# Optimization experiments

Measured on AMD Instinct MI355X. Metric: run time of the kernel, lower is better.

Reference implementation:

```python
import jax, jax.numpy as jnp
import numpy as np

# dims
B, T, N, D = 4, 256, 64, 512
H, DH = 8, 64            # n_head, d_head; H*DH == D
DF = 4 * D               # SwiGLU hidden
EPS = 1e-6


def rmsnorm(x, w):
    return x * jax.lax.rsqrt(jnp.mean(x * x, axis=-1, keepdims=True) + EPS) * w


def phi(x):
    # positive feature map for kernelized (linear) attention ('SMReg' assumed elu+1 style)
    return jax.nn.elu(x) + 1.0


def heads(x):
    return x.reshape(*x.shape[:-1], H, DH)


def lin_att(Xq, Xkv, wq, wk, wv, wo):
    # low-rank high-order linear attention: kernelized attention applied
    # independently along each tensor mode (time T, entities N), averaged.
    q = phi(heads(Xq @ wq))   # [B,T,N,H,DH]
    k = phi(heads(Xkv @ wk))
    v = heads(Xkv @ wv)
    # mode 1 (time): attend over T, batch over (B,N)
    kv_t = jnp.einsum('btnhk,btnhv->bnhkv', k, v)          # [B,N,H,DH,DH]
    ks_t = k.sum(axis=1)                                   # [B,N,H,DH]
    den_t = jnp.einsum('btnhk,bnhk->btnh', q, ks_t) + EPS
    out_t = jnp.einsum('btnhk,bnhkv->btnhv', q, kv_t) / den_t[..., None]
    # mode 2 (entities): attend over N, batch over (B,T)
    kv_n = jnp.einsum('btnhk,btnhv->bthkv', k, v)
    ks_n = k.sum(axis=2)
    den_n = jnp.einsum('btnhk,bthk->btnh', q, ks_n) + EPS
    out_n = jnp.einsum('btnhk,bthkv->btnhv', q, kv_n) / den_n[..., None]
    out = 0.5 * (out_t + out_n)
    return out.reshape(*Xq.shape[:-1], H * DH) @ wo


def swiglu(x, w1, w2, w3):
    return (jax.nn.silu(x @ w1) * (x @ w3)) @ w2


def setup_inputs() -> dict:
    key = jax.random.key(0)
    ks = jax.random.split(key, 20)
    s = 0.02
    inp = {
        'X': jax.random.normal(ks[0], (B, T, N, D), jnp.float32),
        'Z': jax.random.normal(ks[1], (B, T, N, D), jnp.float32),
        'n1': jnp.ones((D,), jnp.float32),
        'n2': jnp.ones((D,), jnp.float32),
        'n3': jnp.ones((D,), jnp.float32),
        'nz': jnp.ones((D,), jnp.float32),
        'a_wq': jax.random.normal(ks[2], (D, H * DH), jnp.float32) * s,
        'a_wk': jax.random.normal(ks[3], (D, H * DH), jnp.float32) * s,
        'a_wv': jax.random.normal(ks[4], (D, H * DH), jnp.float32) * s,
        'a_wo': jax.random.normal(ks[5], (H * DH, D), jnp.float32) * s,
        'c_wq': jax.random.normal(ks[6], (D, H * DH), jnp.float32) * s,
        'c_wk': jax.random.normal(ks[7], (D, H * DH), jnp.float32) * s,
        'c_wv': jax.random.normal(ks[8], (D, H * DH), jnp.float32) * s,
        'c_wo': jax.random.normal(ks[9], (H * DH, D), jnp.float32) * s,
        'f_w1': jax.random.normal(ks[10], (D, DF), jnp.float32) * s,
        'f_w2': jax.random.normal(ks[11], (DF, D), jnp.float32) * s,
        'f_w3': jax.random.normal(ks[12], (D, DF), jnp.float32) * s,
    }
    return inp


def reference(X, Z, n1, n2, n3, nz, a_wq, a_wk, a_wv, a_wo,
              c_wq, c_wk, c_wv, c_wo, f_w1, f_w2, f_w3):
    # h = X + SelfAtt(norm1(X))
    xn = rmsnorm(X, n1)
    h = X + lin_att(xn, xn, a_wq, a_wk, a_wv, a_wo)
    # h = h + CrossAtt(norm3(h), normz(Z))
    h = h + lin_att(rmsnorm(h, n3), rmsnorm(Z, nz), c_wq, c_wk, c_wv, c_wo)
    # out = h + SwiGLU(norm2(h))   (dropout p=0 -> identity)
    return h + swiglu(rmsnorm(h, n2), f_w1, f_w2, f_w3)
```

## Files before the change

kernel.cpp:

```cpp
#include <hip/hip_runtime.h>

typedef short s16x8 __attribute__((ext_vector_type(8)));
typedef float f32x4 __attribute__((ext_vector_type(4)));
typedef unsigned short u16;
typedef unsigned int u32;

__device__ __forceinline__ float bf2f(u16 u) {
  union { unsigned int i; float f; } v; v.i = ((unsigned int)u) << 16; return v.f;
}
__device__ __forceinline__ u16 f2bf(float f) {
  union { float f; unsigned int i; } v; v.f = f;
  unsigned int r = v.i + 0x7fffu + ((v.i >> 16) & 1u);
  return (u16)(r >> 16);
}

__device__ __forceinline__ void gload16(const u16* g, u16* l) {
  __builtin_amdgcn_global_load_lds(
      (const __attribute__((address_space(1))) u32*)g,
      (__attribute__((address_space(3))) u32*)l, 16, 0, 0);
}

template<int KDIM, int NDIM>
__launch_bounds__(256)
__global__ void wprep(const float* __restrict__ in, u16* __restrict__ out) {
  __shared__ float t[64][65];
  const int tid = threadIdx.x;
  const int nb = NDIM / 64;
  const int tk0 = (blockIdx.x / nb) * 64;
  const int tn0 = (blockIdx.x % nb) * 64;
#pragma unroll
  for (int i = 0; i < 16; i++) {
    int idx = i * 256 + tid;
    int r = idx >> 6, c = idx & 63;
    t[r][c] = in[(long)(tk0 + r) * NDIM + (tn0 + c)];
  }
  __syncthreads();
#pragma unroll
  for (int i = 0; i < 16; i++) {
    int idx = i * 256 + tid;
    int nn = idx >> 6, kk = idx & 63;
    out[(long)(tn0 + nn) * KDIM + (tk0 + kk)] = f2bf(t[kk][nn]);
  }
}

__launch_bounds__(256)
__global__ void rmsnorm_f32(const float* __restrict__ x, const float* __restrict__ w,
                            u16* __restrict__ out) {
  const long row = (long)blockIdx.x * 4 + (threadIdx.x >> 6);
  const int lane = threadIdx.x & 63;
  const float* xr = x + row * 512 + lane * 8;
  float4 v0 = *(const float4*)xr;
  float4 v1 = *(const float4*)(xr + 4);
  float ss = v0.x*v0.x + v0.y*v0.y + v0.z*v0.z + v0.w*v0.w
           + v1.x*v1.x + v1.y*v1.y + v1.z*v1.z + v1.w*v1.w;
#pragma unroll
  for (int o = 1; o < 64; o <<= 1) ss += __shfl_xor(ss, o);
  float sc = rsqrtf(ss * (1.0f / 512.0f) + 1e-6f);
  const float* wp = w + lane * 8;
  float4 w0 = *(const float4*)wp;
  float4 w1 = *(const float4*)(wp + 4);
  union { u16 u[8]; uint4 v; } o;
  o.u[0] = f2bf(v0.x * sc * w0.x);
  o.u[1] = f2bf(v0.y * sc * w0.y);
  o.u[2] = f2bf(v0.z * sc * w0.z);
  o.u[3] = f2bf(v0.w * sc * w0.w);
  o.u[4] = f2bf(v1.x * sc * w1.x);
  o.u[5] = f2bf(v1.y * sc * w1.y);
  o.u[6] = f2bf(v1.z * sc * w1.z);
  o.u[7] = f2bf(v1.w * sc * w1.w);
  *(uint4*)(out + row * 512 + lane * 8) = o.v;
}

__launch_bounds__(256)
__global__ void rmsnorm_bf16(const u16* __restrict__ x, const float* __restrict__ w,
                             u16* __restrict__ out) {
  const long row = (long)blockIdx.x * 4 + (threadIdx.x >> 6);
  const int lane = threadIdx.x & 63;
  uint4 u = *(const uint4*)(x + row * 512 + lane * 8);
  const u16* us = (const u16*)&u;
  float f[8];
  float ss = 0.f;
#pragma unroll
  for (int j = 0; j < 8; j++) { f[j] = bf2f(us[j]); ss += f[j] * f[j]; }
#pragma unroll
  for (int o = 1; o < 64; o <<= 1) ss += __shfl_xor(ss, o);
  float sc = rsqrtf(ss * (1.0f / 512.0f) + 1e-6f);
  const float* wp = w + lane * 8;
  union { u16 u[8]; uint4 v; } o;
#pragma unroll
  for (int j = 0; j < 8; j++) o.u[j] = f2bf(f[j] * sc * wp[j]);
  *(uint4*)(out + row * 512 + lane * 8) = o.v;
}

enum { EPI_BF16 = 0, EPI_PHI = 1, EPI_RESX = 2, EPI_RESH = 3, EPI_SILUMUL = 4,
       EPI_OUTF = 5, EPI_QKV = 6, EPI_KV = 7 };

template<int KD, int EPI>
__launch_bounds__(256)
__global__ void gemm128(const u16* __restrict__ A, const u16* __restrict__ Bt,
                        void* __restrict__ C0, void* __restrict__ C1,
                        void* __restrict__ C2, const void* __restrict__ aux,
                        int Ns) {
  __shared__ u16 As[2][128][64];
  __shared__ u16 Bs[2][128][64];
  const int tid = threadIdx.x;
  const int lane = tid & 63;
  const int wv = tid >> 6;
  const int gx = gridDim.x;
  int L = blockIdx.y * gx + blockIdx.x;
  const int cpx = (gx * gridDim.y) >> 3;
  L = (L & 7) * cpx + (L >> 3);
  const long m0 = (long)(L / gx) * 128;
  const int nb = L % gx;
  const long n0 = (long)nb * 128;

  const int wr = (wv >> 1) * 64;
  const int wc = (wv & 1) * 64;
  const int fr = lane & 15;
  const int frq = lane >> 4;

  const int r0 = wv * 32 + (lane >> 3);
  const int sg8 = ((lane & 7) ^ ((lane >> 3) & 7)) * 8;
  const u16* Ag = A + (m0 + r0) * KD + sg8;
  const u16* Bg = Bt + (n0 + r0) * KD + sg8;
  u16* Alds = &As[0][0][0] + wv * 2048;
  u16* Blds = &Bs[0][0][0] + wv * 2048;

  f32x4 acc[4][4] = {};

  auto STAGE = [&](int b, int kt) {
    const long k0 = (long)kt * 64;
#pragma unroll
    for (int j = 0; j < 4; j++) {
      gload16(Ag + (long)(j * 8) * KD + k0, Alds + b * 8192 + j * 512);
      gload16(Bg + (long)(j * 8) * KD + k0, Blds + b * 8192 + j * 512);
    }
  };
  auto COMPUTE = [&](int b) {
#pragma unroll
    for (int ks = 0; ks < 2; ks++) {
      const int slot = ((ks * 4 + frq) ^ (fr & 7)) * 8;
      s16x8 af[4], bf[4];
#pragma unroll
      for (int i = 0; i < 4; i++) af[i] = *(const s16x8*)&As[b][wr + i * 16 + fr][slot];
#pragma unroll
      for (int j = 0; j < 4; j++) bf[j] = *(const s16x8*)&Bs[b][wc + j * 16 + fr][slot];
#pragma unroll
      for (int i = 0; i < 4; i++)
#pragma unroll
        for (int j = 0; j < 4; j++)
          acc[i][j] = __builtin_amdgcn_mfma_f32_16x16x32_bf16(af[i], bf[j], acc[i][j], 0, 0, 0);
    }
  };

  constexpr int NT = KD / 64;
  STAGE(0, 0);
#pragma unroll 1
  for (int t = 0; t < NT; ++t) {
    if (t + 1 < NT) {
      STAGE((t + 1) & 1, t + 1);
      asm volatile("s_waitcnt vmcnt(8)" ::: "memory");
    } else {
      asm volatile("s_waitcnt vmcnt(0)" ::: "memory");
    }
    __builtin_amdgcn_s_barrier();
    COMPUTE(t & 1);
    asm volatile("s_waitcnt lgkmcnt(0)" ::: "memory");
    __builtin_amdgcn_s_barrier();
  }

  const int col = lane & 15;
  const int rb = frq * 4;
#pragma unroll
  for (int i = 0; i < 4; i++) {
#pragma unroll
    for (int r = 0; r < 4; r++) {
      long m = m0 + wr + i * 16 + rb + r;
#pragma unroll
      for (int j = 0; j < 4; j++) {
        long nlocal = wc + j * 16 + col;
        float v = acc[i][j][r];
        if constexpr (EPI == EPI_QKV) {
          int seg = nb >> 2;
          long off = m * 512 + ((n0 + nlocal) & 511);
          u16* P = (u16*)(seg == 0 ? C0 : (seg == 1 ? C1 : C2));
          float p = (seg < 2) ? (v > 0.f ? v + 1.f : __expf(v)) : v;
          P[off] = f2bf(p);
        } else if constexpr (EPI == EPI_KV) {
          int seg = nb >> 2;
          long off = m * 512 + ((n0 + nlocal) & 511);
          u16* P = (u16*)(seg == 0 ? C0 : C1);
          float p = (seg == 0) ? (v > 0.f ? v + 1.f : __expf(v)) : v;
          P[off] = f2bf(p);
        } else {
          long off = m * Ns + (n0 + nlocal);
          if constexpr (EPI == EPI_BF16) {
            ((u16*)C0)[off] = f2bf(v);
          } else if constexpr (EPI == EPI_PHI) {
            float p = v > 0.f ? v + 1.f : __expf(v);
            ((u16*)C0)[off] = f2bf(p);
          } else if constexpr (EPI == EPI_RESX) {
            ((u16*)C0)[off] = f2bf(((const float*)aux)[off] + v);
          } else if constexpr (EPI == EPI_RESH) {
            ((u16*)C0)[off] = f2bf(bf2f(((const u16*)aux)[off]) + v);
          } else if constexpr (EPI == EPI_SILUMUL) {
            float t2 = bf2f(((const u16*)aux)[off]);
            float s = t2 / (1.f + __expf(-t2));
            ((u16*)C0)[off] = f2bf(s * v);
          } else {
            ((float*)C0)[off] = bf2f(((const u16*)aux)[off]) + v;
          }
        }
      }
    }
  }
}

__launch_bounds__(256)
__global__ void att_mode1(const u16* __restrict__ q, const u16* __restrict__ k,
                          const u16* __restrict__ v, u16* __restrict__ attc) {
  __shared__ u16 Ks[128][72];
  __shared__ u16 Vs[128][72];
  __shared__ u16 KVT[64][72];
  __shared__ float ksump[4][64];
  __shared__ float ksum_s[64];
  __shared__ float dinv[256];
  const int tid = threadIdx.x;
  const int lane = tid & 63;
  const int w = tid >> 6;
  const int bnh = blockIdx.x;
  const int h = bnh & 7;
  const int bn = bnh >> 3;
  const int n = bn & 63;
  const int b = bn >> 6;
  const long base = ((long)b * 16384 + n) * 512 + h * 64;
  const int fr = lane & 15;
  const int fk = (lane >> 4) * 8;
  const int sdk = tid & 63, sqq = tid >> 6;

  f32x4 acc[4] = {};
  float ks_acc = 0.f;

  for (int half = 0; half < 2; half++) {
    __syncthreads();
#pragma unroll
    for (int rep = 0; rep < 4; rep++) {
      int idx = rep * 256 + tid;
      int tl = idx >> 3, c8 = idx & 7;
      long go = base + (long)(half * 128 + tl) * 32768 + c8 * 8;
      *(uint4*)&Ks[tl][c8 * 8] = *(const uint4*)(k + go);
      *(uint4*)&Vs[tl][c8 * 8] = *(const uint4*)(v + go);
    }
    __syncthreads();
#pragma unroll
    for (int i = 0; i < 32; i++) ks_acc += bf2f(Ks[sqq * 32 + i][sdk]);
#pragma unroll
    for (int ks = 0; ks < 4; ks++) {
      s16x8 af, bfr[4];
#pragma unroll
      for (int e = 0; e < 8; e++) af[e] = (short)Vs[ks * 32 + fk + e][w * 16 + fr];
#pragma unroll
      for (int j = 0; j < 4; j++)
#pragma unroll
        for (int e = 0; e < 8; e++) bfr[j][e] = (short)Ks[ks * 32 + fk + e][j * 16 + fr];
#pragma unroll
      for (int j = 0; j < 4; j++)
        acc[j] = __builtin_amdgcn_mfma_f32_16x16x32_bf16(af, bfr[j], acc[j], 0, 0, 0);
    }
  }
  ksump[sqq][sdk] = ks_acc;
  __syncthreads();
  {
    const int colL = lane & 15, rb = (lane >> 4) * 4;
#pragma unroll
    for (int j = 0; j < 4; j++)
#pragma unroll
      for (int r = 0; r < 4; r++)
        KVT[w * 16 + rb + r][j * 16 + colL] = f2bf(acc[j][r]);
  }
  if (tid < 64) ksum_s[tid] = ksump[0][tid] + ksump[1][tid] + ksump[2][tid] + ksump[3][tid];
  __syncthreads();
  {
    const u16* qp = q + base + (long)tid * 32768;
    float d = 0.f;
#pragma unroll
    for (int c8 = 0; c8 < 8; c8++) {
      uint4 u = ((const uint4*)qp)[c8];
      const u16* us = (const u16*)&u;
#pragma unroll
      for (int e = 0; e < 8; e++) d += bf2f(us[e]) * ksum_s[c8 * 8 + e];
    }
    dinv[tid] = 0.5f / (d + 1e-6f);
  }
  f32x4 acc2[4][4] = {};
#pragma unroll
  for (int ks = 0; ks < 2; ks++) {
    s16x8 aq[4], bk[4];
#pragma unroll
    for (int i = 0; i < 4; i++)
      aq[i] = *(const s16x8*)(q + base + (long)(w * 64 + i * 16 + fr) * 32768 + ks * 32 + fk);
#pragma unroll
    for (int j = 0; j < 4; j++)
      bk[j] = *(const s16x8*)&KVT[j * 16 + fr][ks * 32 + fk];
#pragma unroll
    for (int i = 0; i < 4; i++)
#pragma unroll
      for (int j = 0; j < 4; j++)
        acc2[i][j] = __builtin_amdgcn_mfma_f32_16x16x32_bf16(aq[i], bk[j], acc2[i][j], 0, 0, 0);
  }
  __syncthreads();
  const int colL = lane & 15, rb = (lane >> 4) * 4;
#pragma unroll
  for (int i = 0; i < 4; i++)
#pragma unroll
    for (int r = 0; r < 4; r++) {
      int t = w * 64 + i * 16 + rb + r;
      float inv = dinv[t];
#pragma unroll
      for (int j = 0; j < 4; j++)
        attc[base + (long)t * 32768 + j * 16 + colL] = f2bf(acc2[i][j][r] * inv);
    }
}

__launch_bounds__(256)
__global__ void att_mode2(const u16* __restrict__ q, const u16* __restrict__ k,
                          const u16* __restrict__ v, u16* __restrict__ attc) {
  __shared__ u16 Ks[64][72];
  __shared__ u16 Vs[64][72];
  __shared__ u16 KVT[64][72];
  __shared__ float ksump[4][64];
  __shared__ float ksum_s[64];
  __shared__ float dinv[64];
  const int tid = threadIdx.x;
  const int lane = tid & 63;
  const int w = tid >> 6;
  const int bth = blockIdx.x;
  const int h = bth & 7;
  const long bt = bth >> 3;
  const long base = bt * 32768 + h * 64;
  const int fr = lane & 15;
  const int fk = (lane >> 4) * 8;
  const int sdk = tid & 63, sqq = tid >> 6;

#pragma unroll
  for (int rep = 0; rep < 2; rep++) {
    int idx = rep * 256 + tid;
    int nl = idx >> 3, c8 = idx & 7;
    long go = base + (long)nl * 512 + c8 * 8;
    *(uint4*)&Ks[nl][c8 * 8] = *(const uint4*)(k + go);
    *(uint4*)&Vs[nl][c8 * 8] = *(const uint4*)(v + go);
  }
  __syncthreads();
  {
    float s = 0.f;
#pragma unroll
    for (int i = 0; i < 16; i++) s += bf2f(Ks[sqq * 16 + i][sdk]);
    ksump[sqq][sdk] = s;
  }
  f32x4 acc[4] = {};
#pragma unroll
  for (int ks = 0; ks < 2; ks++) {
    s16x8 af, bfr[4];
#pragma unroll
    for (int e = 0; e < 8; e++) af[e] = (short)Vs[ks * 32 + fk + e][w * 16 + fr];
#pragma unroll
    for (int j = 0; j < 4; j++)
#pragma unroll
      for (int e = 0; e < 8; e++) bfr[j][e] = (short)Ks[ks * 32 + fk + e][j * 16 + fr];
#pragma unroll
    for (int j = 0; j < 4; j++)
      acc[j] = __builtin_amdgcn_mfma_f32_16x16x32_bf16(af, bfr[j], acc[j], 0, 0, 0);
  }
  __syncthreads();
  {
    const int colL = lane & 15, rb = (lane >> 4) * 4;
#pragma unroll
    for (int j = 0; j < 4; j++)
#pragma unroll
      for (int r = 0; r < 4; r++)
        KVT[w * 16 + rb + r][j * 16 + colL] = f2bf(acc[j][r]);
  }
  if (tid < 64) ksum_s[tid] = ksump[0][tid] + ksump[1][tid] + ksump[2][tid] + ksump[3][tid];
  __syncthreads();
  if (tid < 64) {
    const u16* qp = q + base + (long)tid * 512;
    float d = 0.f;
#pragma unroll
    for (int c8 = 0; c8 < 8; c8++) {
      uint4 u = ((const uint4*)qp)[c8];
      const u16* us = (const u16*)&u;
#pragma unroll
      for (int e = 0; e < 8; e++) d += bf2f(us[e]) * ksum_s[c8 * 8 + e];
    }
    dinv[tid] = 0.5f / (d + 1e-6f);
  }
  f32x4 acc2[4] = {};
#pragma unroll
  for (int ks = 0; ks < 2; ks++) {
    s16x8 aq, bk[4];
    aq = *(const s16x8*)(q + base + (long)(w * 16 + fr) * 512 + ks * 32 + fk);
#pragma unroll
    for (int j = 0; j < 4; j++)
      bk[j] = *(const s16x8*)&KVT[j * 16 + fr][ks * 32 + fk];
#pragma unroll
    for (int j = 0; j < 4; j++)
      acc2[j] = __builtin_amdgcn_mfma_f32_16x16x32_bf16(aq, bk[j], acc2[j], 0, 0, 0);
  }
  __syncthreads();
  const int colL = lane & 15, rb = (lane >> 4) * 4;
#pragma unroll
  for (int r = 0; r < 4; r++) {
    int nr = w * 16 + rb + r;
    float inv = dinv[nr];
#pragma unroll
    for (int j = 0; j < 4; j++) {
      long o = base + (long)nr * 512 + j * 16 + colL;
      attc[o] = f2bf(bf2f(attc[o]) + acc2[j][r] * inv);
    }
  }
}

extern "C" void kernel_launch(void* const* d_in, const int* in_sizes, int n_in,
                              void* d_out, int out_size, void* d_ws, size_t ws_size,
                              hipStream_t stream) {
  const float* X    = (const float*)d_in[0];
  const float* Z    = (const float*)d_in[1];
  const float* n1   = (const float*)d_in[2];
  const float* n2   = (const float*)d_in[3];
  const float* n3   = (const float*)d_in[4];
  const float* nz   = (const float*)d_in[5];
  const float* a_wq = (const float*)d_in[6];
  const float* a_wk = (const float*)d_in[7];
  const float* a_wv = (const float*)d_in[8];
  const float* a_wo = (const float*)d_in[9];
  const float* c_wq = (const float*)d_in[10];
  const float* c_wk = (const float*)d_in[11];
  const float* c_wv = (const float*)d_in[12];
  const float* c_wo = (const float*)d_in[13];
  const float* f_w1 = (const float*)d_in[14];
  const float* f_w2 = (const float*)d_in[15];
  const float* f_w3 = (const float*)d_in[16];
  float* out = (float*)d_out;
  (void)ws_size; (void)in_sizes; (void)n_in; (void)out_size;

  char* p = (char*)d_ws;
  size_t off = 0;
  auto take = [&](size_t bytes) -> char* {
    char* r = p + off;
    off += (bytes + 255) & ~(size_t)255;
    return r;
  };
  u16* w_aq = (u16*)take(512 * 512 * 2);
  u16* w_ak = (u16*)take(512 * 512 * 2);
  u16* w_av = (u16*)take(512 * 512 * 2);
  u16* w_ao = (u16*)take(512 * 512 * 2);
  u16* w_cq = (u16*)take(512 * 512 * 2);
  u16* w_ck = (u16*)take(512 * 512 * 2);
  u16* w_cv = (u16*)take(512 * 512 * 2);
  u16* w_co = (u16*)take(512 * 512 * 2);
  u16* w_f1 = (u16*)take(2048 * 512 * 2);
  u16* w_f3 = (u16*)take(2048 * 512 * 2);
  u16* w_f2 = (u16*)take(512 * 2048 * 2);
  u16* xn   = (u16*)take((size_t)65536 * 512 * 2);
  u16* hbuf = (u16*)take((size_t)65536 * 512 * 2);
  u16* qbuf = (u16*)take((size_t)65536 * 512 * 2);
  u16* kbuf = (u16*)d_out;
  u16* vbuf = (u16*)d_out + (size_t)65536 * 512;
  u16* attc = xn;
  u16* tslot = qbuf;

  dim3 b256(256);
  dim3 gQKV(12, 512);
  dim3 gKV(8, 512);
  dim3 gP(4, 512);
  dim3 gU(16, 128);
  dim3 gD(4, 128);

  wprep<512, 512><<<64, b256, 0, stream>>>(a_wq, w_aq);
  wprep<512, 512><<<64, b256, 0, stream>>>(a_wk, w_ak);
  wprep<512, 512><<<64, b256, 0, stream>>>(a_wv, w_av);
  wprep<512, 512><<<64, b256, 0, stream>>>(a_wo, w_ao);
  wprep<512, 512><<<64, b256, 0, stream>>>(c_wq, w_cq);
  wprep<512, 512><<<64, b256, 0, stream>>>(c_wk, w_ck);
  wprep<512, 512><<<64, b256, 0, stream>>>(c_wv, w_cv);
  wprep<512, 512><<<64, b256, 0, stream>>>(c_wo, w_co);
  wprep<512, 2048><<<256, b256, 0, stream>>>(f_w1, w_f1);
  wprep<512, 2048><<<256, b256, 0, stream>>>(f_w3, w_f3);
  wprep<2048, 512><<<256, b256, 0, stream>>>(f_w2, w_f2);

  rmsnorm_f32<<<16384, b256, 0, stream>>>(X, n1, xn);
  gemm128<512, EPI_QKV><<<gQKV, b256, 0, stream>>>(xn, w_aq, qbuf, kbuf, vbuf, nullptr, 1536);
  att_mode1<<<2048, b256, 0, stream>>>(qbuf, kbuf, vbuf, attc);
  att_mode2<<<8192, b256, 0, stream>>>(qbuf, kbuf, vbuf, attc);
  gemm128<512, EPI_RESX><<<gP, b256, 0, stream>>>(attc, w_ao, hbuf, nullptr, nullptr, X, 512);

  rmsnorm_bf16<<<16384, b256, 0, stream>>>(hbuf, n3, xn);
  gemm128<512, EPI_PHI><<<gP, b256, 0, stream>>>(xn, w_cq, qbuf, nullptr, nullptr, nullptr, 512);
  rmsnorm_f32<<<16384, b256, 0, stream>>>(Z, nz, xn);
  gemm128<512, EPI_KV><<<gKV, b256, 0, stream>>>(xn, w_ck, kbuf, vbuf, nullptr, nullptr, 1024);
  att_mode1<<<2048, b256, 0, stream>>>(qbuf, kbuf, vbuf, attc);
  att_mode2<<<8192, b256, 0, stream>>>(qbuf, kbuf, vbuf, attc);
  gemm128<512, EPI_RESH><<<gP, b256, 0, stream>>>(attc, w_co, hbuf, nullptr, nullptr, hbuf, 512);

  rmsnorm_bf16<<<16384, b256, 0, stream>>>(hbuf, n2, xn);
  const int CH = 16384;
  for (int c = 0; c < 4; c++) {
    const size_t ro = (size_t)c * CH * 512;
    gemm128<512, EPI_BF16><<<gU, b256, 0, stream>>>(xn + ro, w_f1, tslot, nullptr, nullptr, nullptr, 2048);
    gemm128<512, EPI_SILUMUL><<<gU, b256, 0, stream>>>(xn + ro, w_f3, tslot, nullptr, nullptr, tslot, 2048);
    gemm128<2048, EPI_OUTF><<<gD, b256, 0, stream>>>(tslot, w_f2, out + ro, nullptr, nullptr, hbuf + ro, 512);
  }
}
```

Baseline: 1.498 ms.

## Enlarge GEMM tiles to 256x256 with 8 waves and 4-stage LDS pipeline

Replaces the 128x128 GEMM kernel (4 waves, 2-stage, K-step 64) with a 256x256 tile using 8 waves, each computing a 128x64 sub-tile, with a 4-buffer LDS ring and K-step 32 prefetched two stages ahead. The larger tile raises arithmetic intensity and cuts global/L2 traffic per FLOP, and s_setprio is raised around the MFMA block. In exchange it uses more accumulator registers (32 f32x4 per lane) and 64KB of LDS, which lowers occupancy and gives fewer workgroups per launch.

Result: slower. 1.771 ms (+18.2%).

```diff
diff --git a/kernel.cpp b/kernel.cpp
--- a/kernel.cpp
+++ b/kernel.cpp
@@ -96,98 +96,104 @@
        EPI_OUTF = 5, EPI_QKV = 6, EPI_KV = 7 };
 
 template<int KD, int EPI>
-__launch_bounds__(256)
-__global__ void gemm128(const u16* __restrict__ A, const u16* __restrict__ Bt,
+__launch_bounds__(512)
+__global__ void gemm256(const u16* __restrict__ A, const u16* __restrict__ Bt,
                         void* __restrict__ C0, void* __restrict__ C1,
                         void* __restrict__ C2, const void* __restrict__ aux,
                         int Ns) {
-  __shared__ u16 As[2][128][64];
-  __shared__ u16 Bs[2][128][64];
+  __shared__ u16 As[4][256][32];
+  __shared__ u16 Bs[4][256][32];
   const int tid = threadIdx.x;
   const int lane = tid & 63;
-  const int wv = tid >> 6;
+  const int wid = tid >> 6;
   const int gx = gridDim.x;
   int L = blockIdx.y * gx + blockIdx.x;
   const int cpx = (gx * gridDim.y) >> 3;
   L = (L & 7) * cpx + (L >> 3);
-  const long m0 = (long)(L / gx) * 128;
+  const long m0 = (long)(L / gx) * 256;
   const int nb = L % gx;
-  const long n0 = (long)nb * 128;
-
-  const int wr = (wv >> 1) * 64;
-  const int wc = (wv & 1) * 64;
+  const long n0 = (long)nb * 256;
+
+  const int wrbase = (wid >> 2) * 128;
+  const int wcbase = (wid & 3) * 64;
   const int fr = lane & 15;
   const int frq = lane >> 4;
 
-  const int r0 = wv * 32 + (lane >> 3);
-  const int sg8 = ((lane & 7) ^ ((lane >> 3) & 7)) * 8;
-  const u16* Ag = A + (m0 + r0) * KD + sg8;
-  const u16* Bg = Bt + (n0 + r0) * KD + sg8;
-  u16* Alds = &As[0][0][0] + wv * 2048;
-  u16* Blds = &Bs[0][0][0] + wv * 2048;
-
-  f32x4 acc[4][4] = {};
-
-  auto STAGE = [&](int b, int kt) {
-    const long k0 = (long)kt * 64;
-#pragma unroll
-    for (int j = 0; j < 4; j++) {
-      gload16(Ag + (long)(j * 8) * KD + k0, Alds + b * 8192 + j * 512);
-      gload16(Bg + (long)(j * 8) * KD + k0, Blds + b * 8192 + j * 512);
-    }
+  const int srow = lane >> 2;
+  const int sslot = ((lane & 3) ^ (srow & 3)) * 8;
+  const u16* Ag = A + (m0 + wid * 32 + srow) * KD + sslot;
+  const u16* Bg = Bt + (n0 + wid * 32 + srow) * KD + sslot;
+  u16* Al = &As[0][0][0] + wid * 1024;
+  u16* Bl = &Bs[0][0][0] + wid * 1024;
+
+  f32x4 acc[8][4] = {};
+
+  auto STAGE = [&](int t) {
+    const int b = t & 3;
+    const long k0 = (long)t * 32;
+    gload16(Ag + k0, Al + b * 8192);
+    gload16(Ag + (long)16 * KD + k0, Al + b * 8192 + 512);
+    gload16(Bg + k0, Bl + b * 8192);
+    gload16(Bg + (long)16 * KD + k0, Bl + b * 8192 + 512);
   };
   auto COMPUTE = [&](int b) {
-#pragma unroll
-    for (int ks = 0; ks < 2; ks++) {
-      const int slot = ((ks * 4 + frq) ^ (fr & 7)) * 8;
-      s16x8 af[4], bf[4];
-#pragma unroll
-      for (int i = 0; i < 4; i++) af[i] = *(const s16x8*)&As[b][wr + i * 16 + fr][slot];
-#pragma unroll
-      for (int j = 0; j < 4; j++) bf[j] = *(const s16x8*)&Bs[b][wc + j * 16 + fr][slot];
-#pragma unroll
-      for (int i = 0; i < 4; i++)
-#pragma unroll
-        for (int j = 0; j < 4; j++)
-          acc[i][j] = __builtin_amdgcn_mfma_f32_16x16x32_bf16(af[i], bf[j], acc[i][j], 0, 0, 0);
-    }
+    s16x8 af[8], bf[4];
+#pragma unroll
+    for (int i = 0; i < 8; i++) {
+      const int row = wrbase + i * 16 + fr;
+      af[i] = *(const s16x8*)&As[b][row][(frq ^ (row & 3)) * 8];
+    }
+#pragma unroll
+    for (int j = 0; j < 4; j++) {
+      const int row = wcbase + j * 16 + fr;
+      bf[j] = *(const s16x8*)&Bs[b][row][(frq ^ (row & 3)) * 8];
+    }
+    __builtin_amdgcn_s_setprio(1);
+#pragma unroll
+    for (int i = 0; i < 8; i++)
+#pragma unroll
+      for (int j = 0; j < 4; j++)
+        acc[i][j] = __builtin_amdgcn_mfma_f32_16x16x32_bf16(af[i], bf[j], acc[i][j], 0, 0, 0);
+    __builtin_amdgcn_s_setprio(0);
   };
 
-  constexpr int NT = KD / 64;
-  STAGE(0, 0);
+  constexpr int NT = KD / 32;
+  STAGE(0);
+  STAGE(1);
 #pragma unroll 1
   for (int t = 0; t < NT; ++t) {
-    if (t + 1 < NT) {
-      STAGE((t + 1) & 1, t + 1);
+    if (t + 2 < NT) {
+      STAGE(t + 2);
       asm volatile("s_waitcnt vmcnt(8)" ::: "memory");
+    } else if (t + 1 < NT) {
+      asm volatile("s_waitcnt vmcnt(4)" ::: "memory");
     } else {
       asm volatile("s_waitcnt vmcnt(0)" ::: "memory");
     }
     __builtin_amdgcn_s_barrier();
-    COMPUTE(t & 1);
-    asm volatile("s_waitcnt lgkmcnt(0)" ::: "memory");
+    COMPUTE(t & 3);
     __builtin_amdgcn_s_barrier();
   }
 
   const int col = lane & 15;
   const int rb = frq * 4;
 #pragma unroll
-  for (int i = 0; i < 4; i++) {
+  for (int i = 0; i < 8; i++) {
 #pragma unroll
     for (int r = 0; r < 4; r++) {
-      long m = m0 + wr + i * 16 + rb + r;
+      long m = m0 + wrbase + i * 16 + rb + r;
 #pragma unroll
       for (int j = 0; j < 4; j++) {
-        long nlocal = wc + j * 16 + col;
+        long nlocal = wcbase + j * 16 + col;
         float v = acc[i][j][r];
         if constexpr (EPI == EPI_QKV) {
-          int seg = nb >> 2;
+          int seg = nb >> 1;
           long off = m * 512 + ((n0 + nlocal) & 511);
           u16* P = (u16*)(seg == 0 ? C0 : (seg == 1 ? C1 : C2));
           float p = (seg < 2) ? (v > 0.f ? v + 1.f : __expf(v)) : v;
           P[off] = f2bf(p);
         } else if constexpr (EPI == EPI_KV) {
-          int seg = nb >> 2;
+          int seg = nb >> 1;
           long off = m * 512 + ((n0 + nlocal) & 511);
           u16* P = (u16*)(seg == 0 ? C0 : C1);
           float p = (seg == 0) ? (v > 0.f ? v + 1.f : __expf(v)) : v;
@@ -470,11 +476,12 @@
   u16* tslot = qbuf;
 
   dim3 b256(256);
-  dim3 gQKV(12, 512);
-  dim3 gKV(8, 512);
-  dim3 gP(4, 512);
-  dim3 gU(16, 128);
-  dim3 gD(4, 128);
+  dim3 b512(512);
+  dim3 gQKV(6, 256);
+  dim3 gKV(4, 256);
+  dim3 gP(2, 256);
+  dim3 gU(8, 64);
+  dim3 gD(2, 64);
 
   wprep<512, 512><<<64, b256, 0, stream>>>(a_wq, w_aq);
   wprep<512, 512><<<64, b256, 0, stream>>>(a_wk, w_ak);
@@ -489,25 +496,25 @@
   wprep<2048, 512><<<256, b256, 0, stream>>>(f_w2, w_f2);
 
   rmsnorm_f32<<<16384, b256, 0, stream>>>(X, n1, xn);
-  gemm128<512, EPI_QKV><<<gQKV, b256, 0, stream>>>(xn, w_aq, qbuf, kbuf, vbuf, nullptr, 1536);
+  gemm256<512, EPI_QKV><<<gQKV, b512, 0, stream>>>(xn, w_aq, qbuf, kbuf, vbuf, nullptr, 1536);
   att_mode1<<<2048, b256, 0, stream>>>(qbuf, kbuf, vbuf, attc);
   att_mode2<<<8192, b256, 0, stream>>>(qbuf, kbuf, vbuf, attc);
-  gemm128<512, EPI_RESX><<<gP, b256, 0, stream>>>(attc, w_ao, hbuf, nullptr, nullptr, X, 512);
+  gemm256<512, EPI_RESX><<<gP, b512, 0, stream>>>(attc, w_ao, hbuf, nullptr, nullptr, X, 512);
 
   rmsnorm_bf16<<<16384, b256, 0, stream>>>(hbuf, n3, xn);
-  gemm128<512, EPI_PHI><<<gP, b256, 0, stream>>>(xn, w_cq, qbuf, nullptr, nullptr, nullptr, 512);
+  gemm256<512, EPI_PHI><<<gP, b512, 0, stream>>>(xn, w_cq, qbuf, nullptr, nullptr, nullptr, 512);
   rmsnorm_f32<<<16384, b256, 0, stream>>>(Z, nz, xn);
-  gemm128<512, EPI_KV><<<gKV, b256, 0, stream>>>(xn, w_ck, kbuf, vbuf, nullptr, nullptr, 1024);
+  gemm256<512, EPI_KV><<<gKV, b512, 0, stream>>>(xn, w_ck, kbuf, vbuf, nullptr, nullptr, 1024);
   att_mode1<<<2048, b256, 0, stream>>>(qbuf, kbuf, vbuf, attc);
   att_mode2<<<8192, b256, 0, stream>>>(qbuf, kbuf, vbuf, attc);
-  gemm128<512, EPI_RESH><<<gP, b256, 0, stream>>>(attc, w_co, hbuf, nullptr, nullptr, hbuf, 512);
+  gemm256<512, EPI_RESH><<<gP, b512, 0, stream>>>(attc, w_co, hbuf, nullptr, nullptr, hbuf, 512);
 
   rmsnorm_bf16<<<16384, b256, 0, stream>>>(hbuf, n2, xn);
   const int CH = 16384;
   for (int c = 0; c < 4; c++) {
     const size_t ro = (size_t)c * CH * 512;
-    gemm128<512, EPI_BF16><<<gU, b256, 0, stream>>>(xn + ro, w_f1, tslot, nullptr, nullptr, nullptr, 2048);
-    gemm128<512, EPI_SILUMUL><<<gU, b256, 0, stream>>>(xn + ro, w_f3, tslot, nullptr, nullptr, tslot, 2048);
-    gemm128<2048, EPI_OUTF><<<gD, b256, 0, stream>>>(tslot, w_f2, out + ro, nullptr, nullptr, hbuf + ro, 512);
-  }
-}
+    gemm256<512, EPI_BF16><<<gU, b512, 0, stream>>>(xn + ro, w_f1, tslot, nullptr, nullptr, nullptr, 2048);
+    gemm256<512, EPI_SILUMUL><<<gU, b512, 0, stream>>>(xn + ro, w_f3, tslot, nullptr, nullptr, tslot, 2048);
+    gemm256<2048, EPI_OUTF><<<gD, b512, 0, stream>>>(tslot, w_f2, out + ro, nullptr, nullptr, hbuf + ro, 512);
+  }
+}
```

## Store K/V transposed and pair-packed in LDS for vectorized MFMA fragment loads

Applied to the files above, without the earlier changes.

In both attention kernels, K and V tiles are now transposed into LDS as u32 words, each packing two consecutive time or entity elements. MFMA operand fragments and the key-sum reductions can then use 128-bit LDS reads instead of eight scalar u16 gathers per fragment. Mode 1 now loads all 256 timesteps in one pass instead of two halves, which removes a sync loop but uses more LDS per block and may lower occupancy. The transposing scatter stores into LDS may cause bank conflicts.

New measurement: 1.518 ms. No clear change (+1.4%).

```diff
diff --git a/kernel.cpp b/kernel.cpp
--- a/kernel.cpp
+++ b/kernel.cpp
@@ -12,6 +12,12 @@
   union { float f; unsigned int i; } v; v.f = f;
   unsigned int r = v.i + 0x7fffu + ((v.i >> 16) & 1u);
   return (u16)(r >> 16);
+}
+__device__ __forceinline__ float bflo(u32 x) {
+  union { unsigned int i; float f; } v; v.i = x << 16; return v.f;
+}
+__device__ __forceinline__ float bfhi(u32 x) {
+  union { unsigned int i; float f; } v; v.i = x & 0xffff0000u; return v.f;
 }
 
 __device__ __forceinline__ void gload16(const u16* g, u16* l) {
@@ -219,8 +225,8 @@
 __launch_bounds__(256)
 __global__ void att_mode1(const u16* __restrict__ q, const u16* __restrict__ k,
                           const u16* __restrict__ v, u16* __restrict__ attc) {
-  __shared__ u16 Ks[128][72];
-  __shared__ u16 Vs[128][72];
+  __shared__ u32 KT[64][132];
+  __shared__ u32 VT[64][132];
   __shared__ u16 KVT[64][72];
   __shared__ float ksump[4][64];
   __shared__ float ksum_s[64];
@@ -235,43 +241,55 @@
   const int b = bn >> 6;
   const long base = ((long)b * 16384 + n) * 512 + h * 64;
   const int fr = lane & 15;
-  const int fk = (lane >> 4) * 8;
-  const int sdk = tid & 63, sqq = tid >> 6;
+  const int frq = lane >> 4;
+  const int fk = frq * 8;
+
+#pragma unroll
+  for (int r = 0; r < 4; r++) {
+    const int tp = (tid & 63) + (r & 1) * 64;
+    const int c8 = (tid >> 6) + (r >> 1) * 4;
+    const long g0 = base + (long)(2 * tp) * 32768 + c8 * 8;
+    uint4 ka = *(const uint4*)(k + g0);
+    uint4 kb = *(const uint4*)(k + g0 + 32768);
+    uint4 va = *(const uint4*)(v + g0);
+    uint4 vb = *(const uint4*)(v + g0 + 32768);
+    const u16* kap = (const u16*)&ka; const u16* kbp = (const u16*)&kb;
+    const u16* vap = (const u16*)&va; const u16* vbp = (const u16*)&vb;
+#pragma unroll
+    for (int e = 0; e < 8; e++) {
+      KT[c8 * 8 + e][tp] = (u32)kap[e] | ((u32)kbp[e] << 16);
+      VT[c8 * 8 + e][tp] = (u32)vap[e] | ((u32)vbp[e] << 16);
+    }
+  }
+  __syncthreads();
+
+  {
+    const int dk = tid >> 2, qq = tid & 3;
+    float s = 0.f;
+#pragma unroll
+    for (int i = 0; i < 8; i++) {
+      uint4 x = *(const uint4*)&KT[dk][qq * 32 + i * 4];
+      s += bflo(x.x) + bfhi(x.x) + bflo(x.y) + bfhi(x.y)
+         + bflo(x.z) + bfhi(x.z) + bflo(x.w) + bfhi(x.w);
+    }
+    ksump[qq][dk] = s;
+  }
 
   f32x4 acc[4] = {};
-  float ks_acc = 0.f;
-
-  for (int half = 0; half < 2; half++) {
-    __syncthreads();
-#pragma unroll
-    for (int rep = 0; rep < 4; rep++) {
-      int idx = rep * 256 + tid;
-      int tl = idx >> 3, c8 = idx & 7;
-      long go = base + (long)(half * 128 + tl) * 32768 + c8 * 8;
-      *(uint4*)&Ks[tl][c8 * 8] = *(const uint4*)(k + go);
-      *(uint4*)&Vs[tl][c8 * 8] = *(const uint4*)(v + go);
-    }
-    __syncthreads();
-#pragma unroll
-    for (int i = 0; i < 32; i++) ks_acc += bf2f(Ks[sqq * 32 + i][sdk]);
-#pragma unroll
-    for (int ks = 0; ks < 4; ks++) {
-      s16x8 af, bfr[4];
-#pragma unroll
-      for (int e = 0; e < 8; e++) af[e] = (short)Vs[ks * 32 + fk + e][w * 16 + fr];
-#pragma unroll
-      for (int j = 0; j < 4; j++)
-#pragma unroll
-        for (int e = 0; e < 8; e++) bfr[j][e] = (short)Ks[ks * 32 + fk + e][j * 16 + fr];
-#pragma unroll
-      for (int j = 0; j < 4; j++)
-        acc[j] = __builtin_amdgcn_mfma_f32_16x16x32_bf16(af, bfr[j], acc[j], 0, 0, 0);
-    }
-  }
-  ksump[sqq][sdk] = ks_acc;
+#pragma unroll
+  for (int ks = 0; ks < 8; ks++) {
+    s16x8 af = *(const s16x8*)&VT[w * 16 + fr][ks * 16 + frq * 4];
+    s16x8 bk[4];
+#pragma unroll
+    for (int j = 0; j < 4; j++)
+      bk[j] = *(const s16x8*)&KT[j * 16 + fr][ks * 16 + frq * 4];
+#pragma unroll
+    for (int j = 0; j < 4; j++)
+      acc[j] = __builtin_amdgcn_mfma_f32_16x16x32_bf16(af, bk[j], acc[j], 0, 0, 0);
+  }
   __syncthreads();
   {
-    const int colL = lane & 15, rb = (lane >> 4) * 4;
+    const int colL = lane & 15, rb = frq * 4;
 #pragma unroll
     for (int j = 0; j < 4; j++)
 #pragma unroll
@@ -309,7 +327,7 @@
         acc2[i][j] = __builtin_amdgcn_mfma_f32_16x16x32_bf16(aq[i], bk[j], acc2[i][j], 0, 0, 0);
   }
   __syncthreads();
-  const int colL = lane & 15, rb = (lane >> 4) * 4;
+  const int colL = lane & 15, rb = frq * 4;
 #pragma unroll
   for (int i = 0; i < 4; i++)
 #pragma unroll
@@ -325,8 +343,8 @@
 __launch_bounds__(256)
 __global__ void att_mode2(const u16* __restrict__ q, const u16* __restrict__ k,
                           const u16* __restrict__ v, u16* __restrict__ attc) {
-  __shared__ u16 Ks[64][72];
-  __shared__ u16 Vs[64][72];
+  __shared__ u32 KT[64][36];
+  __shared__ u32 VT[64][36];
   __shared__ u16 KVT[64][72];
   __shared__ float ksump[4][64];
   __shared__ float ksum_s[64];
@@ -339,41 +357,51 @@
   const long bt = bth >> 3;
   const long base = bt * 32768 + h * 64;
   const int fr = lane & 15;
-  const int fk = (lane >> 4) * 8;
-  const int sdk = tid & 63, sqq = tid >> 6;
-
-#pragma unroll
-  for (int rep = 0; rep < 2; rep++) {
-    int idx = rep * 256 + tid;
-    int nl = idx >> 3, c8 = idx & 7;
-    long go = base + (long)nl * 512 + c8 * 8;
-    *(uint4*)&Ks[nl][c8 * 8] = *(const uint4*)(k + go);
-    *(uint4*)&Vs[nl][c8 * 8] = *(const uint4*)(v + go);
-  }
-  __syncthreads();
+  const int frq = lane >> 4;
+  const int fk = frq * 8;
+
   {
-    float s = 0.f;
-#pragma unroll
-    for (int i = 0; i < 16; i++) s += bf2f(Ks[sqq * 16 + i][sdk]);
-    ksump[sqq][sdk] = s;
+    const int np = tid & 31;
+    const int c8 = tid >> 5;
+    const long g0 = base + (long)(2 * np) * 512 + c8 * 8;
+    uint4 ka = *(const uint4*)(k + g0);
+    uint4 kb = *(const uint4*)(k + g0 + 512);
+    uint4 va = *(const uint4*)(v + g0);
+    uint4 vb = *(const uint4*)(v + g0 + 512);
+    const u16* kap = (const u16*)&ka; const u16* kbp = (const u16*)&kb;
+    const u16* vap = (const u16*)&va; const u16* vbp = (const u16*)&vb;
+#pragma unroll
+    for (int e = 0; e < 8; e++) {
+      KT[c8 * 8 + e][np] = (u32)kap[e] | ((u32)kbp[e] << 16);
+      VT[c8 * 8 + e][np] = (u32)vap[e] | ((u32)vbp[e] << 16);
+    }
+  }
+  __syncthreads();
+  {
+    const int dk = tid >> 2, qq = tid & 3;
+    uint4 x0 = *(const uint4*)&KT[dk][qq * 8];
+    uint4 x1 = *(const uint4*)&KT[dk][qq * 8 + 4];
+    float s = bflo(x0.x) + bfhi(x0.x) + bflo(x0.y) + bfhi(x0.y)
+            + bflo(x0.z) + bfhi(x0.z) + bflo(x0.w) + bfhi(x0.w)
+            + bflo(x1.x) + bfhi(x1.x) + bflo(x1.y) + bfhi(x1.y)
+            + bflo(x1.z) + bfhi(x1.z) + bflo(x1.w) + bfhi(x1.w);
+    ksump[qq][dk] = s;
   }
   f32x4 acc[4] = {};
 #pragma unroll
   for (int ks = 0; ks < 2; ks++) {
-    s16x8 af, bfr[4];
-#pragma unroll
-    for (int e = 0; e < 8; e++) af[e] = (short)Vs[ks * 32 + fk + e][w * 16 + fr];
-#pragma unroll
-    for (int j = 0; j < 4; j++)
-#pragma unroll
-      for (int e = 0; e < 8; e++) bfr[j][e] = (short)Ks[ks * 32 + fk + e][j * 16 + fr];
-#pragma unroll
-    for (int j = 0; j < 4; j++)
-      acc[j] = __builtin_amdgcn_mfma_f32_16x16x32_bf16(af, bfr[j], acc[j], 0, 0, 0);
+    s16x8 af = *(const s16x8*)&VT[w * 16 + fr][ks * 16 + frq * 4];
+    s16x8 bk[4];
+#pragma unroll
+    for (int j = 0; j < 4; j++)
+      bk[j] = *(const s16x8*)&KT[j * 16 + fr][ks * 16 + frq * 4];
+#pragma unroll
+    for (int j = 0; j < 4; j++)
+      acc[j] = __builtin_amdgcn_mfma_f32_16x16x32_bf16(af, bk[j], acc[j], 0, 0, 0);
   }
   __syncthreads();
   {
-    const int colL = lane & 15, rb = (lane >> 4) * 4;
+    const int colL = lane & 15, rb = frq * 4;
 #pragma unroll
     for (int j = 0; j < 4; j++)
 #pragma unroll
@@ -407,7 +435,7 @@
       acc2[j] = __builtin_amdgcn_mfma_f32_16x16x32_bf16(aq, bk[j], acc2[j], 0, 0, 0);
   }
   __syncthreads();
-  const int colL = lane & 15, rb = (lane >> 4) * 4;
+  const int colL = lane & 15, rb = frq * 4;
 #pragma unroll
   for (int r = 0; r < 4; r++) {
     int nr = w * 16 + rb + r;
```
